# Kernel optimization log

Hardware: AMD Instinct MI355X
Metric: run time of the kernel (lower is better)

The kernel has to match this reference:

```python
import jax, jax.numpy as jnp
import numpy as np


def _gcn_layer(x, W, b, src, dst, norm, n_nodes):
    # x: [N, Fin]; transform first (PyG GCNConv): h = x @ W
    h = x @ W  # [N, Fout]
    # gather-scale-scatter: out[d] += norm_e * h[s] over edges (incl. self loops)
    msgs = h[src] * norm[:, None]  # [E+N, Fout]
    agg = jax.ops.segment_sum(msgs, dst, num_segments=n_nodes)
    return agg + b


def setup_inputs() -> dict:
    key = jax.random.key(0)
    k1, k2, k3, k4 = jax.random.split(key, 4)
    N, E, F_IN, HID, OUT = 50000, 800000, 128, 256, 128
    x = jax.random.normal(k1, (N, F_IN), dtype=jnp.float32)
    edge_index = jax.random.randint(k2, (2, E), 0, N, dtype=jnp.int64)
    W1 = jax.random.normal(k3, (F_IN, HID), dtype=jnp.float32) / np.sqrt(F_IN)
    b1 = jnp.zeros((HID,), dtype=jnp.float32)
    W2 = jax.random.normal(k4, (HID, OUT), dtype=jnp.float32) / np.sqrt(HID)
    b2 = jnp.zeros((OUT,), dtype=jnp.float32)
    return {"x": x, "edge_index": edge_index, "W1": W1, "b1": b1, "W2": W2, "b2": b2}


def reference(x, edge_index, W1, b1, W2, b2):
    N = x.shape[0]
    # GCN normalization with self loops: A_hat = D^-1/2 (A + I) D^-1/2
    self_loops = jnp.arange(N, dtype=edge_index.dtype)
    src = jnp.concatenate([edge_index[0], self_loops])
    dst = jnp.concatenate([edge_index[1], self_loops])
    deg = jax.ops.segment_sum(jnp.ones_like(dst, dtype=x.dtype), dst, num_segments=N)
    dinv = jnp.where(deg > 0, jax.lax.rsqrt(deg), 0.0)
    norm = dinv[src] * dinv[dst]  # [E+N]
    h = _gcn_layer(x, W1, b1, src, dst, norm, N)
    h = jax.nn.relu(h)  # dropout is identity in eval mode
    out = _gcn_layer(h, W2, b2, src, dst, norm, N)
    return out  # unsupervised mode returns raw embeddings [N, 128]
```

## Files before the change

kernel.cpp:

```cpp
#include <hip/hip_runtime.h>
#include <hip/hip_bf16.h>


static constexpr int N_NODES = 50000;
static constexpr int N_EDGES = 800000;
static constexpr int F_IN = 128;
static constexpr int HID  = 256;
static constexpr int F_OUT = 128;

typedef __attribute__((ext_vector_type(8))) short short8;
typedef __attribute__((ext_vector_type(4))) float f32x4;

__device__ __forceinline__ unsigned short f2bf(float f) {
    union { float f; unsigned u; } x; x.f = f;
    unsigned r = x.u + 0x7FFF + ((x.u >> 16) & 1);
    return (unsigned short)(r >> 16);
}
__device__ __forceinline__ float bf2f(unsigned short h) {
    union { unsigned u; float f; } x; x.u = ((unsigned)h) << 16;
    return x.f;
}

__global__ void deg_pos_kernel(const int* __restrict__ dst, int* __restrict__ deg,
                               int* __restrict__ pos, int E) {
    int i = blockIdx.x * blockDim.x + threadIdx.x;
    if (i < E) pos[i] = atomicAdd(&deg[dst[i]], 1);
}

__global__ void dinv_kernel(const int* __restrict__ deg, float* __restrict__ dinv, int N) {
    int i = blockIdx.x * blockDim.x + threadIdx.x;
    if (i < N) dinv[i] = rsqrtf((float)(deg[i] + 1));
}

__global__ __launch_bounds__(256) void scan_reduce(const int* __restrict__ deg,
                                                   int* __restrict__ bsums, int N) {
    int i = blockIdx.x * 256 + threadIdx.x;
    int v = (i < N) ? deg[i] : 0;
#pragma unroll
    for (int ofs = 32; ofs > 0; ofs >>= 1) v += __shfl_down(v, ofs);
    __shared__ int ws[4];
    if ((threadIdx.x & 63) == 0) ws[threadIdx.x >> 6] = v;
    __syncthreads();
    if (threadIdx.x == 0) bsums[blockIdx.x] = ws[0] + ws[1] + ws[2] + ws[3];
}

__global__ __launch_bounds__(256) void scan_bsums(int* __restrict__ bsums, int nb) {
    __shared__ int s[256];
    int tid = threadIdx.x;
    s[tid] = (tid < nb) ? bsums[tid] : 0;
    __syncthreads();
    for (int ofs = 1; ofs < 256; ofs <<= 1) {
        int v = (tid >= ofs) ? s[tid - ofs] : 0;
        __syncthreads();
        s[tid] += v;
        __syncthreads();
    }
    bsums[tid] = (tid == 0) ? 0 : s[tid - 1];
}

__global__ __launch_bounds__(256) void scan_final(const int* __restrict__ deg,
                                                  const int* __restrict__ bsums,
                                                  int* __restrict__ off, int N) {
    __shared__ int s[256];
    const int tid = threadIdx.x;
    const int i = blockIdx.x * 256 + tid;
    int v = (i < N) ? deg[i] : 0;
    s[tid] = v;
    __syncthreads();
    for (int ofs = 1; ofs < 256; ofs <<= 1) {
        int t = (tid >= ofs) ? s[tid - ofs] : 0;
        __syncthreads();
        s[tid] += t;
        __syncthreads();
    }
    int excl = (tid == 0) ? 0 : s[tid - 1];
    if (i <= N) off[i] = bsums[blockIdx.x] + excl;
}

__global__ void scatter_kernel(const int* __restrict__ src, const int* __restrict__ dst,
                               const int* __restrict__ pos, const int* __restrict__ off,
                               int* __restrict__ csr, int E) {
    int i = blockIdx.x * blockDim.x + threadIdx.x;
    if (i < E) csr[off[dst[i]] + pos[i]] = src[i];
}

__global__ void scalex_kernel(const float* __restrict__ x, const float* __restrict__ dinv,
                              unsigned short* __restrict__ xs, int n8) {
    int i = blockIdx.x * blockDim.x + threadIdx.x;
    if (i < n8) {
        float dv = dinv[i >> 4];
        float4 v0 = ((const float4*)x)[i * 2];
        float4 v1 = ((const float4*)x)[i * 2 + 1];
        short8 o;
        o[0] = (short)f2bf(v0.x * dv); o[1] = (short)f2bf(v0.y * dv);
        o[2] = (short)f2bf(v0.z * dv); o[3] = (short)f2bf(v0.w * dv);
        o[4] = (short)f2bf(v1.x * dv); o[5] = (short)f2bf(v1.y * dv);
        o[6] = (short)f2bf(v1.z * dv); o[7] = (short)f2bf(v1.w * dv);
        *(short8*)(xs + (size_t)i * 8) = o;
    }
}

__global__ void wt_kernel(const float* __restrict__ W, unsigned short* __restrict__ WT,
                          int K, int N) {
    int t = blockIdx.x * blockDim.x + threadIdx.x;
    if (t < K * N) {
        int n = t / K, k = t - n * K;
        WT[t] = f2bf(W[(size_t)k * N + n]);
    }
}

template <int MODE>
__global__ __launch_bounds__(256) void agg_bf16(const unsigned short* __restrict__ hs,
                                                const int* __restrict__ off,
                                                const int* __restrict__ csr,
                                                const float* __restrict__ dinv,
                                                const float* __restrict__ bias,
                                                void* __restrict__ outp, int N) {
    const int wid = threadIdx.x >> 6;
    const int n = blockIdx.x * 4 + wid;
    if (n >= N) return;
    const int lane = threadIdx.x & 63;
    const int lane16 = lane & 15;
    const int slot = lane >> 4;

    float va[8], vb[8], vc[8], vd[8];
#pragma unroll
    for (int j = 0; j < 8; j++) { va[j] = 0.f; vb[j] = 0.f; vc[j] = 0.f; vd[j] = 0.f; }

    if (slot == 0) {
        short8 s = *(const short8*)(hs + (size_t)n * 128 + lane16 * 8);
#pragma unroll
        for (int j = 0; j < 8; j++) va[j] = bf2f((unsigned short)s[j]);
    }

    const int e1 = off[n + 1];
    int e = off[n] + slot;
    for (; e + 12 < e1; e += 16) {
        int s0 = csr[e];
        int s1 = csr[e + 4];
        int s2 = csr[e + 8];
        int s3 = csr[e + 12];
        short8 v0 = *(const short8*)(hs + (size_t)s0 * 128 + lane16 * 8);
        short8 v1 = *(const short8*)(hs + (size_t)s1 * 128 + lane16 * 8);
        short8 v2 = *(const short8*)(hs + (size_t)s2 * 128 + lane16 * 8);
        short8 v3 = *(const short8*)(hs + (size_t)s3 * 128 + lane16 * 8);
#pragma unroll
        for (int j = 0; j < 8; j++) va[j] += bf2f((unsigned short)v0[j]);
#pragma unroll
        for (int j = 0; j < 8; j++) vb[j] += bf2f((unsigned short)v1[j]);
#pragma unroll
        for (int j = 0; j < 8; j++) vc[j] += bf2f((unsigned short)v2[j]);
#pragma unroll
        for (int j = 0; j < 8; j++) vd[j] += bf2f((unsigned short)v3[j]);
    }
    for (; e < e1; e += 4) {
        int s0 = csr[e];
        short8 v0 = *(const short8*)(hs + (size_t)s0 * 128 + lane16 * 8);
#pragma unroll
        for (int j = 0; j < 8; j++) va[j] += bf2f((unsigned short)v0[j]);
    }
#pragma unroll
    for (int j = 0; j < 8; j++) va[j] += vb[j] + vc[j] + vd[j];

#pragma unroll
    for (int j = 0; j < 8; j++) va[j] += __shfl_down(va[j], 32);
#pragma unroll
    for (int j = 0; j < 8; j++) va[j] += __shfl_down(va[j], 16);

    if (lane < 16) {
        float dv = dinv[n];
        if (MODE == 0) {
            short8 o;
#pragma unroll
            for (int j = 0; j < 8; j++) o[j] = (short)f2bf(va[j] * dv);
            *(short8*)((unsigned short*)outp + (size_t)n * 128 + lane * 8) = o;
        } else {
            float* op = (float*)outp + (size_t)n * 128 + lane * 8;
            float4 o0, o1;
            o0.x = va[0] * dv + bias[lane * 8 + 0];
            o0.y = va[1] * dv + bias[lane * 8 + 1];
            o0.z = va[2] * dv + bias[lane * 8 + 2];
            o0.w = va[3] * dv + bias[lane * 8 + 3];
            o1.x = va[4] * dv + bias[lane * 8 + 4];
            o1.y = va[5] * dv + bias[lane * 8 + 5];
            o1.z = va[6] * dv + bias[lane * 8 + 6];
            o1.w = va[7] * dv + bias[lane * 8 + 7];
            ((float4*)op)[0] = o0;
            ((float4*)op)[1] = o1;
        }
    }
}

template <int K, int NC, int EPI>
__global__ __launch_bounds__(256) void mfma_gemm(const unsigned short* __restrict__ X,
                                                 const unsigned short* __restrict__ WT,
                                                 const float* __restrict__ bias,
                                                 const float* __restrict__ dinv,
                                                 unsigned short* __restrict__ out, int M) {
    constexpr int KC = K / 32;
    constexpr int TILES = NC / 32;
    const int wid = threadIdx.x >> 6;
    const int lane = threadIdx.x & 63;
    const int an = lane & 15;
    const int q = lane >> 4;
    const int rowgrp = wid & 1;
    const int colgrp = wid >> 1;
    const int m0 = blockIdx.x * 64 + rowgrp * 32;
    const int ntbase = colgrp * TILES;

    short8 a[2][KC];
#pragma unroll
    for (int r = 0; r < 2; r++) {
        int row = m0 + r * 16 + an;
        if (row >= M) row = M - 1;
        const unsigned short* xp = X + (size_t)row * K + q * 8;
#pragma unroll
        for (int c = 0; c < KC; c++) a[r][c] = *(const short8*)(xp + c * 32);
    }

    auto do_tile = [&](int t) {
        const int col = (ntbase + t) * 16 + an;
        const unsigned short* wp = WT + (size_t)col * K + q * 8;
        short8 b[KC];
#pragma unroll
        for (int c = 0; c < KC; c++) b[c] = *(const short8*)(wp + c * 32);
        f32x4 acc0 = {0.f, 0.f, 0.f, 0.f};
        f32x4 acc1 = {0.f, 0.f, 0.f, 0.f};
#pragma unroll
        for (int c = 0; c < KC; c++) {
            acc0 = __builtin_amdgcn_mfma_f32_16x16x32_bf16(a[0][c], b[c], acc0, 0, 0, 0);
            acc1 = __builtin_amdgcn_mfma_f32_16x16x32_bf16(a[1][c], b[c], acc1, 0, 0, 0);
        }
        float bv = (EPI == 1) ? bias[col] : 0.f;
#pragma unroll
        for (int rr = 0; rr < 4; rr++) {
            int m = m0 + q * 4 + rr;
            if (m < M) {
                float v = acc0[rr];
                if (EPI == 1) v = fmaxf(v + bv, 0.f);
                else v *= dinv[m];
                out[(size_t)m * NC + col] = f2bf(v);
            }
            int m2 = m0 + 16 + q * 4 + rr;
            if (m2 < M) {
                float v = acc1[rr];
                if (EPI == 1) v = fmaxf(v + bv, 0.f);
                else v *= dinv[m2];
                out[(size_t)m2 * NC + col] = f2bf(v);
            }
        }
    };

    if constexpr (K == 128) {
#pragma unroll 4
        for (int t = 0; t < TILES; t++) do_tile(t);
    } else {
#pragma unroll 2
        for (int t = 0; t < TILES; t++) do_tile(t);
    }
}

extern "C" void kernel_launch(void* const* d_in, const int* in_sizes, int n_in,
                              void* d_out, int out_size, void* d_ws, size_t ws_size,
                              hipStream_t stream) {
    const float* x  = (const float*)d_in[0];
    const int*   ei = (const int*)d_in[1];
    const float* W1 = (const float*)d_in[2];
    const float* b1 = (const float*)d_in[3];
    const float* W2 = (const float*)d_in[4];
    const float* b2 = (const float*)d_in[5];

    const int N = N_NODES;
    const int E = N_EDGES;
    const int* srcp = ei;
    const int* dstp = ei + E;

    char* base = (char*)d_ws;
    size_t o = 0;
    auto alloc = [&](size_t bytes) {
        void* p = base + o;
        o = (o + bytes + 255) & ~(size_t)255;
        return p;
    };
    int*            deg  = (int*)alloc((size_t)N * 4);
    int*            offs = (int*)alloc((size_t)(N + 1) * 4);
    float*          dinv = (float*)alloc((size_t)N * 4);
    int*            bsum = (int*)alloc(256 * 4);
    int*            pos  = (int*)alloc((size_t)E * 4);
    int*            csr  = (int*)alloc((size_t)E * 4);
    unsigned short* xs   = (unsigned short*)alloc((size_t)N * F_IN * 2);
    unsigned short* Y    = (unsigned short*)alloc((size_t)N * F_IN * 2);
    unsigned short* h2   = (unsigned short*)alloc((size_t)N * HID * 2);
    unsigned short* w1t  = (unsigned short*)alloc((size_t)F_IN * HID * 2);
    unsigned short* w2t  = (unsigned short*)alloc((size_t)HID * F_OUT * 2);
    unsigned short* hs2  = xs;

    hipMemsetAsync(deg, 0, (size_t)N * 4, stream);

    const int NB = (N + 256) / 256;
    deg_pos_kernel<<<(E + 255) / 256, 256, 0, stream>>>(dstp, deg, pos, E);
    dinv_kernel<<<(N + 255) / 256, 256, 0, stream>>>(deg, dinv, N);
    scan_reduce<<<NB, 256, 0, stream>>>(deg, bsum, N);
    scan_bsums<<<1, 256, 0, stream>>>(bsum, NB);
    scan_final<<<NB, 256, 0, stream>>>(deg, bsum, offs, N);
    scatter_kernel<<<(E + 255) / 256, 256, 0, stream>>>(srcp, dstp, pos, offs, csr, E);
    scalex_kernel<<<(N * F_IN / 8 + 255) / 256, 256, 0, stream>>>(x, dinv, xs, N * F_IN / 8);
    wt_kernel<<<(F_IN * HID + 255) / 256, 256, 0, stream>>>(W1, w1t, F_IN, HID);
    wt_kernel<<<(HID * F_OUT + 255) / 256, 256, 0, stream>>>(W2, w2t, HID, F_OUT);

    agg_bf16<0><<<(N + 3) / 4, 256, 0, stream>>>(xs, offs, csr, dinv, nullptr, Y, N);
    mfma_gemm<F_IN, HID, 1><<<(N + 63) / 64, 256, 0, stream>>>(Y, w1t, b1, nullptr, h2, N);

    mfma_gemm<HID, F_OUT, 0><<<(N + 63) / 64, 256, 0, stream>>>(h2, w2t, nullptr, dinv, hs2, N);
    agg_bf16<1><<<(N + 3) / 4, 256, 0, stream>>>(hs2, offs, csr, dinv, b2, d_out, N);
}
```

Baseline: 280.1 us.

## Fuse preprocessing kernels and predicate aggregation tail into unrolled loop

Measured after the change: 263.6 us. 5.9% less time.

```diff
diff --git a/kernel.cpp b/kernel.cpp
--- a/kernel.cpp
+++ b/kernel.cpp
@@ -27,15 +27,12 @@
     if (i < E) pos[i] = atomicAdd(&deg[dst[i]], 1);
 }
 
-__global__ void dinv_kernel(const int* __restrict__ deg, float* __restrict__ dinv, int N) {
-    int i = blockIdx.x * blockDim.x + threadIdx.x;
-    if (i < N) dinv[i] = rsqrtf((float)(deg[i] + 1));
-}
-
-__global__ __launch_bounds__(256) void scan_reduce(const int* __restrict__ deg,
-                                                   int* __restrict__ bsums, int N) {
+__global__ __launch_bounds__(256) void scan_reduce_dinv(const int* __restrict__ deg,
+                                                        int* __restrict__ bsums,
+                                                        float* __restrict__ dinv, int N) {
     int i = blockIdx.x * 256 + threadIdx.x;
     int v = (i < N) ? deg[i] : 0;
+    if (i < N) dinv[i] = rsqrtf((float)(v + 1));
 #pragma unroll
     for (int ofs = 32; ofs > 0; ofs >>= 1) v += __shfl_down(v, ofs);
     __shared__ int ws[4];
@@ -44,37 +41,28 @@
     if (threadIdx.x == 0) bsums[blockIdx.x] = ws[0] + ws[1] + ws[2] + ws[3];
 }
 
-__global__ __launch_bounds__(256) void scan_bsums(int* __restrict__ bsums, int nb) {
-    __shared__ int s[256];
-    int tid = threadIdx.x;
-    s[tid] = (tid < nb) ? bsums[tid] : 0;
-    __syncthreads();
-    for (int ofs = 1; ofs < 256; ofs <<= 1) {
-        int v = (tid >= ofs) ? s[tid - ofs] : 0;
-        __syncthreads();
-        s[tid] += v;
-        __syncthreads();
-    }
-    bsums[tid] = (tid == 0) ? 0 : s[tid - 1];
-}
-
 __global__ __launch_bounds__(256) void scan_final(const int* __restrict__ deg,
                                                   const int* __restrict__ bsums,
-                                                  int* __restrict__ off, int N) {
+                                                  int* __restrict__ off, int N, int nb) {
+    __shared__ int bs[256];
     __shared__ int s[256];
     const int tid = threadIdx.x;
+    bs[tid] = (tid < nb) ? bsums[tid] : 0;
     const int i = blockIdx.x * 256 + tid;
     int v = (i < N) ? deg[i] : 0;
     s[tid] = v;
     __syncthreads();
     for (int ofs = 1; ofs < 256; ofs <<= 1) {
-        int t = (tid >= ofs) ? s[tid - ofs] : 0;
+        int tb = (tid >= ofs) ? bs[tid - ofs] : 0;
+        int tv = (tid >= ofs) ? s[tid - ofs] : 0;
         __syncthreads();
-        s[tid] += t;
+        bs[tid] += tb;
+        s[tid] += tv;
         __syncthreads();
     }
+    int bbase = (blockIdx.x == 0) ? 0 : bs[blockIdx.x - 1];
     int excl = (tid == 0) ? 0 : s[tid - 1];
-    if (i <= N) off[i] = bsums[blockIdx.x] + excl;
+    if (i <= N) off[i] = bbase + excl;
 }
 
 __global__ void scatter_kernel(const int* __restrict__ src, const int* __restrict__ dst,
@@ -84,28 +72,37 @@
     if (i < E) csr[off[dst[i]] + pos[i]] = src[i];
 }
 
-__global__ void scalex_kernel(const float* __restrict__ x, const float* __restrict__ dinv,
-                              unsigned short* __restrict__ xs, int n8) {
-    int i = blockIdx.x * blockDim.x + threadIdx.x;
-    if (i < n8) {
-        float dv = dinv[i >> 4];
-        float4 v0 = ((const float4*)x)[i * 2];
-        float4 v1 = ((const float4*)x)[i * 2 + 1];
-        short8 o;
-        o[0] = (short)f2bf(v0.x * dv); o[1] = (short)f2bf(v0.y * dv);
-        o[2] = (short)f2bf(v0.z * dv); o[3] = (short)f2bf(v0.w * dv);
-        o[4] = (short)f2bf(v1.x * dv); o[5] = (short)f2bf(v1.y * dv);
-        o[6] = (short)f2bf(v1.z * dv); o[7] = (short)f2bf(v1.w * dv);
-        *(short8*)(xs + (size_t)i * 8) = o;
-    }
-}
-
-__global__ void wt_kernel(const float* __restrict__ W, unsigned short* __restrict__ WT,
-                          int K, int N) {
-    int t = blockIdx.x * blockDim.x + threadIdx.x;
-    if (t < K * N) {
-        int n = t / K, k = t - n * K;
-        WT[t] = f2bf(W[(size_t)k * N + n]);
+__global__ void prep_kernel(const float* __restrict__ x, const float* __restrict__ dinv,
+                            unsigned short* __restrict__ xs,
+                            const float* __restrict__ W1, unsigned short* __restrict__ w1t,
+                            const float* __restrict__ W2, unsigned short* __restrict__ w2t,
+                            int NBX, int NB1) {
+    const int b = blockIdx.x;
+    if (b < NBX) {
+        int i = b * 256 + threadIdx.x;
+        if (i < N_NODES * F_IN / 8) {
+            float dv = dinv[i >> 4];
+            float4 v0 = ((const float4*)x)[i * 2];
+            float4 v1 = ((const float4*)x)[i * 2 + 1];
+            short8 o;
+            o[0] = (short)f2bf(v0.x * dv); o[1] = (short)f2bf(v0.y * dv);
+            o[2] = (short)f2bf(v0.z * dv); o[3] = (short)f2bf(v0.w * dv);
+            o[4] = (short)f2bf(v1.x * dv); o[5] = (short)f2bf(v1.y * dv);
+            o[6] = (short)f2bf(v1.z * dv); o[7] = (short)f2bf(v1.w * dv);
+            *(short8*)(xs + (size_t)i * 8) = o;
+        }
+    } else if (b < NBX + NB1) {
+        int t = (b - NBX) * 256 + threadIdx.x;
+        if (t < F_IN * HID) {
+            int n = t / F_IN, k = t - n * F_IN;
+            w1t[t] = f2bf(W1[(size_t)k * HID + n]);
+        }
+    } else {
+        int t = (b - NBX - NB1) * 256 + threadIdx.x;
+        if (t < HID * F_OUT) {
+            int n = t / HID, k = t - n * HID;
+            w2t[t] = f2bf(W2[(size_t)k * F_OUT + n]);
+        }
     }
 }
 
@@ -133,13 +130,18 @@
         for (int j = 0; j < 8; j++) va[j] = bf2f((unsigned short)s[j]);
     }
 
+    const int e0 = off[n];
     const int e1 = off[n + 1];
-    int e = off[n] + slot;
-    for (; e + 12 < e1; e += 16) {
+    for (int e = e0 + slot; e < e1; e += 16) {
+        const int i1 = e + 4, i2 = e + 8, i3 = e + 12;
+        const float f1 = (i1 < e1) ? 1.f : 0.f;
+        const float f2 = (i2 < e1) ? 1.f : 0.f;
+        const float f3 = (i3 < e1) ? 1.f : 0.f;
+        const int c1 = min(i1, e1 - 1), c2 = min(i2, e1 - 1), c3 = min(i3, e1 - 1);
         int s0 = csr[e];
-        int s1 = csr[e + 4];
-        int s2 = csr[e + 8];
-        int s3 = csr[e + 12];
+        int s1 = csr[c1];
+        int s2 = csr[c2];
+        int s3 = csr[c3];
         short8 v0 = *(const short8*)(hs + (size_t)s0 * 128 + lane16 * 8);
         short8 v1 = *(const short8*)(hs + (size_t)s1 * 128 + lane16 * 8);
         short8 v2 = *(const short8*)(hs + (size_t)s2 * 128 + lane16 * 8);
@@ -147,17 +149,11 @@
 #pragma unroll
         for (int j = 0; j < 8; j++) va[j] += bf2f((unsigned short)v0[j]);
 #pragma unroll
-        for (int j = 0; j < 8; j++) vb[j] += bf2f((unsigned short)v1[j]);
-#pragma unroll
-        for (int j = 0; j < 8; j++) vc[j] += bf2f((unsigned short)v2[j]);
-#pragma unroll
-        for (int j = 0; j < 8; j++) vd[j] += bf2f((unsigned short)v3[j]);
-    }
-    for (; e < e1; e += 4) {
-        int s0 = csr[e];
-        short8 v0 = *(const short8*)(hs + (size_t)s0 * 128 + lane16 * 8);
-#pragma unroll
-        for (int j = 0; j < 8; j++) va[j] += bf2f((unsigned short)v0[j]);
+        for (int j = 0; j < 8; j++) vb[j] = fmaf(f1, bf2f((unsigned short)v1[j]), vb[j]);
+#pragma unroll
+        for (int j = 0; j < 8; j++) vc[j] = fmaf(f2, bf2f((unsigned short)v2[j]), vc[j]);
+#pragma unroll
+        for (int j = 0; j < 8; j++) vd[j] = fmaf(f3, bf2f((unsigned short)v3[j]), vd[j]);
     }
 #pragma unroll
     for (int j = 0; j < 8; j++) va[j] += vb[j] + vc[j] + vd[j];
@@ -298,15 +294,15 @@
     hipMemsetAsync(deg, 0, (size_t)N * 4, stream);
 
     const int NB = (N + 256) / 256;
+    const int NBX = (N * F_IN / 8 + 255) / 256;
+    const int NB1 = (F_IN * HID + 255) / 256;
+    const int NB2 = (HID * F_OUT + 255) / 256;
+
     deg_pos_kernel<<<(E + 255) / 256, 256, 0, stream>>>(dstp, deg, pos, E);
-    dinv_kernel<<<(N + 255) / 256, 256, 0, stream>>>(deg, dinv, N);
-    scan_reduce<<<NB, 256, 0, stream>>>(deg, bsum, N);
-    scan_bsums<<<1, 256, 0, stream>>>(bsum, NB);
-    scan_final<<<NB, 256, 0, stream>>>(deg, bsum, offs, N);
+    scan_reduce_dinv<<<NB, 256, 0, stream>>>(deg, bsum, dinv, N);
+    scan_final<<<NB, 256, 0, stream>>>(deg, bsum, offs, N, NB);
     scatter_kernel<<<(E + 255) / 256, 256, 0, stream>>>(srcp, dstp, pos, offs, csr, E);
-    scalex_kernel<<<(N * F_IN / 8 + 255) / 256, 256, 0, stream>>>(x, dinv, xs, N * F_IN / 8);
-    wt_kernel<<<(F_IN * HID + 255) / 256, 256, 0, stream>>>(W1, w1t, F_IN, HID);
-    wt_kernel<<<(HID * F_OUT + 255) / 256, 256, 0, stream>>>(W2, w2t, HID, F_OUT);
+    prep_kernel<<<NBX + NB1 + NB2, 256, 0, stream>>>(x, dinv, xs, W1, w1t, W2, w2t, NBX, NB1);
 
     agg_bf16<0><<<(N + 3) / 4, 256, 0, stream>>>(xs, offs, csr, dinv, nullptr, Y, N);
     mfma_gemm<F_IN, HID, 1><<<(N + 63) / 64, 256, 0, stream>>>(Y, w1t, b1, nullptr, h2, N);
```
